# Kernel optimization log

Measured on AMD Instinct MI355X. Metric: run time of the kernel, lower is better.

Reference implementation:

```python
import jax, jax.numpy as jnp
import numpy as np
from jax import lax

BLOCK_SIZE = 7
DROP_PROB = 0.1


def setup_inputs() -> dict:
    key = jax.random.key(0)
    kx, ku = jax.random.split(key)
    N, C, H, W = 64, 256, 64, 64
    x = jax.random.normal(kx, (N, C, H, W), dtype=jnp.float32)
    # one uniform draw per valid top-left block position, shared over N and C
    u = jax.random.uniform(ku, (H - BLOCK_SIZE + 1, W - BLOCK_SIZE + 1), dtype=jnp.float32)
    return {"x": x, "u": u}


def _block_mask(u, h, w):
    # drop[i,j] = 1 -> block with top-left (i,j) is dropped
    drop = (u < DROP_PROB).astype(jnp.float32)  # [h-bs+1, w-bs+1]
    # dilate: a pixel (y,x) is zeroed if ANY block covering it was dropped.
    # max-pool with window=bs, stride=1, pad=bs-1 on both sides -> [h, w]
    pad = BLOCK_SIZE - 1
    dilated = lax.reduce_window(
        drop, 0.0, lax.max,
        window_dimensions=(BLOCK_SIZE, BLOCK_SIZE),
        window_strides=(1, 1),
        padding=((pad, pad), (pad, pad)),
    )
    return 1.0 - dilated  # [h, w], 1 = keep


def reference(x, u):
    _, _, h, w = x.shape
    mask = _block_mask(u, h, w)                       # [h, w]
    scale = (h * w) / mask.sum()                      # numel/sum ratio (N,C cancel)
    return x * (mask * scale)[None, None, :, :]
```

## Files before the change

### kernel.cpp

```cpp
#include <hip/hip_runtime.h>

#define BS 7
#define DROPP 0.1f
#define H 64
#define W 64
#define UH (H - BS + 1)
#define UW (W - BS + 1)

__global__ __launch_bounds__(1024) void dropblock_mask_kernel(
    const float* __restrict__ u, float* __restrict__ m)
{
    __shared__ float su[UH * UW];
    __shared__ float ssum[16];
    __shared__ float sscale;

    const int tid = threadIdx.x;
    for (int i = tid; i < UH * UW; i += 1024) su[i] = u[i];
    __syncthreads();

    float mv[4];
    float local = 0.0f;
    #pragma unroll
    for (int k = 0; k < 4; ++k) {
        const int p = tid * 4 + k;
        const int y = p >> 6;
        const int x = p & 63;
        const int i0 = (y - 6 > 0) ? (y - 6) : 0;
        const int i1 = (y < UH - 1) ? y : (UH - 1);
        const int j0 = (x - 6 > 0) ? (x - 6) : 0;
        const int j1 = (x < UW - 1) ? x : (UW - 1);
        float keep = 1.0f;
        for (int i = i0; i <= i1; ++i)
            for (int j = j0; j <= j1; ++j)
                if (su[i * UW + j] < DROPP) keep = 0.0f;
        mv[k] = keep;
        local += keep;
    }

    #pragma unroll
    for (int off = 32; off >= 1; off >>= 1)
        local += __shfl_down(local, off, 64);
    const int wave = tid >> 6;
    const int lane = tid & 63;
    if (lane == 0) ssum[wave] = local;
    __syncthreads();
    if (tid == 0) {
        float tot = 0.0f;
        #pragma unroll
        for (int wv = 0; wv < 16; ++wv) tot += ssum[wv];
        sscale = (float)(H * W) / tot;
    }
    __syncthreads();

    const float s = sscale;
    #pragma unroll
    for (int k = 0; k < 4; ++k)
        m[tid * 4 + k] = mv[k] * s;
}

__global__ __launch_bounds__(256) void dropblock_apply_kernel(
    const float4* __restrict__ x, const float* __restrict__ m,
    float4* __restrict__ out)
{
    const int gid = blockIdx.x * 256 + threadIdx.x;
    const float4* m4 = (const float4*)m;
    const float4 xv = x[gid];
    const float4 mv = m4[gid & 1023];
    float4 ov;
    ov.x = xv.x * mv.x;
    ov.y = xv.y * mv.y;
    ov.z = xv.z * mv.z;
    ov.w = xv.w * mv.w;
    out[gid] = ov;
}

extern "C" void kernel_launch(void* const* d_in, const int* in_sizes, int n_in,
                              void* d_out, int out_size, void* d_ws, size_t ws_size,
                              hipStream_t stream) {
    const float* x = (const float*)d_in[0];
    const float* u = (const float*)d_in[1];
    float* out = (float*)d_out;
    float* m   = (float*)d_ws;

    dropblock_mask_kernel<<<1, 1024, 0, stream>>>(u, m);

    const int total4 = out_size / 4;
    dropblock_apply_kernel<<<total4 / 256, 256, 0, stream>>>(
        (const float4*)x, m, (float4*)out);
}
```

Measured before the change: 428.4 us.

## Compute dropblock mask with ballot bitmasks and use nontemporal loads/stores

The mask kernel now packs drop decisions into 64-bit row bitmasks with ballot, dilates horizontally with shifts/ORs and vertically by OR-ing rows, and counts kept pixels with popcount, replacing the per-pixel 7x7 shared-memory scan. The apply kernel uses native vector types and nontemporal load/store builtins for the streamed x and output. This targets the serial single-block mask cost and cache pollution in the streaming pass; nontemporal hints may or may not help bandwidth on this hardware.

```diff
diff --git a/kernel.cpp b/kernel.cpp
--- a/kernel.cpp
+++ b/kernel.cpp
@@ -2,76 +2,75 @@
 
 #define BS 7
 #define DROPP 0.1f
-#define H 64
-#define W 64
-#define UH (H - BS + 1)
-#define UW (W - BS + 1)
+#define UH 58
+#define UW 58
+
+typedef float f32x4 __attribute__((ext_vector_type(4)));
 
 __global__ __launch_bounds__(1024) void dropblock_mask_kernel(
     const float* __restrict__ u, float* __restrict__ m)
 {
-    __shared__ float su[UH * UW];
-    __shared__ float ssum[16];
+    __shared__ unsigned long long sD[64];
+    __shared__ unsigned long long sR[64];
+    __shared__ unsigned long long sDil[64];
     __shared__ float sscale;
 
-    const int tid = threadIdx.x;
-    for (int i = tid; i < UH * UW; i += 1024) su[i] = u[i];
+    const int tid  = threadIdx.x;
+    const int wave = tid >> 6;
+    const int lane = tid & 63;
+
+    for (int i = wave; i < 64; i += 16) {
+        bool d = false;
+        if (i < UH && lane < UW) d = (u[i * UW + lane] < DROPP);
+        unsigned long long D = __ballot(d);
+        if (lane == 0) sD[i] = D;
+    }
     __syncthreads();
 
-    float mv[4];
-    float local = 0.0f;
-    #pragma unroll
-    for (int k = 0; k < 4; ++k) {
-        const int p = tid * 4 + k;
-        const int y = p >> 6;
-        const int x = p & 63;
+    if (wave == 0) {
+        unsigned long long D = sD[lane];
+        unsigned long long R = D;
+        #pragma unroll
+        for (int s = 1; s <= 6; ++s) R |= (D << s);
+        sR[lane] = R;
+    }
+    __syncthreads();
+
+    if (wave == 0) {
+        const int y = lane;
         const int i0 = (y - 6 > 0) ? (y - 6) : 0;
         const int i1 = (y < UH - 1) ? y : (UH - 1);
-        const int j0 = (x - 6 > 0) ? (x - 6) : 0;
-        const int j1 = (x < UW - 1) ? x : (UW - 1);
-        float keep = 1.0f;
-        for (int i = i0; i <= i1; ++i)
-            for (int j = j0; j <= j1; ++j)
-                if (su[i * UW + j] < DROPP) keep = 0.0f;
-        mv[k] = keep;
-        local += keep;
-    }
-
-    #pragma unroll
-    for (int off = 32; off >= 1; off >>= 1)
-        local += __shfl_down(local, off, 64);
-    const int wave = tid >> 6;
-    const int lane = tid & 63;
-    if (lane == 0) ssum[wave] = local;
-    __syncthreads();
-    if (tid == 0) {
-        float tot = 0.0f;
+        unsigned long long dil = 0ull;
+        for (int i = i0; i <= i1; ++i) dil |= sR[i];
+        sDil[y] = dil;
+        float kept = (float)(64 - __popcll(dil));
         #pragma unroll
-        for (int wv = 0; wv < 16; ++wv) tot += ssum[wv];
-        sscale = (float)(H * W) / tot;
+        for (int off = 32; off >= 1; off >>= 1)
+            kept += __shfl_down(kept, off, 64);
+        if (lane == 0) sscale = 4096.0f / kept;
     }
     __syncthreads();
 
     const float s = sscale;
-    #pragma unroll
-    for (int k = 0; k < 4; ++k)
-        m[tid * 4 + k] = mv[k] * s;
+    const unsigned long long dil = sDil[(tid >> 4) & 63];
+    const int xb = (tid * 4) & 63;
+    f32x4 mv;
+    mv.x = ((dil >> (xb + 0)) & 1ull) ? 0.0f : s;
+    mv.y = ((dil >> (xb + 1)) & 1ull) ? 0.0f : s;
+    mv.z = ((dil >> (xb + 2)) & 1ull) ? 0.0f : s;
+    mv.w = ((dil >> (xb + 3)) & 1ull) ? 0.0f : s;
+    ((f32x4*)m)[tid] = mv;
 }
 
 __global__ __launch_bounds__(256) void dropblock_apply_kernel(
-    const float4* __restrict__ x, const float* __restrict__ m,
-    float4* __restrict__ out)
+    const f32x4* __restrict__ x, const f32x4* __restrict__ m4,
+    f32x4* __restrict__ out)
 {
     const int gid = blockIdx.x * 256 + threadIdx.x;
-    const float4* m4 = (const float4*)m;
-    const float4 xv = x[gid];
-    const float4 mv = m4[gid & 1023];
-    float4 ov;
-    ov.x = xv.x * mv.x;
-    ov.y = xv.y * mv.y;
-    ov.z = xv.z * mv.z;
-    ov.w = xv.w * mv.w;
-    out[gid] = ov;
+    const f32x4 xv = __builtin_nontemporal_load(&x[gid]);
+    const f32x4 mv = m4[gid & 1023];
+    f32x4 ov = xv * mv;
+    __builtin_nontemporal_store(ov, &out[gid]);
 }
 
 extern "C" void kernel_launch(void* const* d_in, const int* in_sizes, int n_in,
@@ -86,5 +85,5 @@
 
     const int total4 = out_size / 4;
     dropblock_apply_kernel<<<total4 / 256, 256, 0, stream>>>(
-        (const float4*)x, m, (float4*)out);
+        (const f32x4*)x, (const f32x4*)m, (f32x4*)out);
 }
```

New measurement: 416.3 us. 1.03x faster.
